# Optimization experiments

Measured on AMD Instinct MI355X. Metric: run time of the kernel, lower is better.

## Reference

```python
import jax, jax.numpy as jnp
import numpy as np

IN_FEATURES = 4096
OUT_FEATURES = 11008
TOKENS = 8


def setup_inputs() -> dict:
    key = jax.random.key(0)
    k_x, k_w, k_s, k_b = jax.random.split(key, 4)
    x = jax.random.normal(k_x, (TOKENS, IN_FEATURES), dtype=jnp.float32)
    # int8-valued quantized weights stored as int32 for portability
    weight_quantized = jax.random.randint(k_w, (OUT_FEATURES, IN_FEATURES), -128, 128, dtype=jnp.int32)
    # per-channel scales (positive, small), shape (out, 1)
    weight_scale = jax.random.uniform(k_s, (OUT_FEATURES, 1), dtype=jnp.float32, minval=1e-4, maxval=2e-2)
    # symmetric quantization -> zero points are zero
    weight_zero_point = jnp.zeros((OUT_FEATURES, 1), dtype=jnp.int32)
    bias = jax.random.normal(k_b, (OUT_FEATURES,), dtype=jnp.float32)
    return {
        "x": x,
        "weight_quantized": weight_quantized,
        "weight_scale": weight_scale,
        "weight_zero_point": weight_zero_point,
        "bias": bias,
    }


def reference(x, weight_quantized, weight_scale, weight_zero_point, bias):
    # Dequantize: (q - zp) * scale, per output channel  -> [out, in] fp32
    w_fp = (weight_quantized.astype(jnp.float32) - weight_zero_point.astype(jnp.float32)) * weight_scale
    # F.linear: x @ W^T + b  -> [tokens, out]
    out = jnp.einsum("ti,oi->to", x, w_fp) + bias
    return out
```

## Files before the change

### kernel.cpp

```cpp
#include <hip/hip_runtime.h>
#include <hip/hip_bf16.h>


constexpr int K_IN  = 4096;
constexpr int N_OUT = 11008;
constexpr int KQ    = K_IN / 4;
constexpr int ITERS = KQ / (64 * 4);

__global__ __launch_bounds__(256) void qlin_kernel(
    const float* __restrict__ x,
    const int*   __restrict__ q,
    const float* __restrict__ scale,
    const int*   __restrict__ zp,
    const float* __restrict__ bias,
    float*       __restrict__ out)
{
    __shared__ float partial[3][64];

    const int tid  = threadIdx.x;
    const int lane = tid & 63;
    const int w    = tid >> 6;
    const int obase = blockIdx.x * 8;
    const int kbase = w * KQ;

    float acc[64];
    #pragma unroll
    for (int i = 0; i < 64; ++i) acc[i] = 0.0f;
    float xs[8];
    #pragma unroll
    for (int t = 0; t < 8; ++t) xs[t] = 0.0f;

    #pragma unroll 2
    for (int it = 0; it < ITERS; ++it) {
        const int k0 = kbase + it * 256 + lane * 4;

        float4 xv[8];
        #pragma unroll
        for (int t = 0; t < 8; ++t)
            xv[t] = *reinterpret_cast<const float4*>(&x[t * K_IN + k0]);

        int4 qv[8];
        #pragma unroll
        for (int c = 0; c < 8; ++c)
            qv[c] = *reinterpret_cast<const int4*>(&q[(obase + c) * K_IN + k0]);

        #pragma unroll
        for (int c = 0; c < 8; ++c) {
            const float q0 = (float)qv[c].x;
            const float q1 = (float)qv[c].y;
            const float q2 = (float)qv[c].z;
            const float q3 = (float)qv[c].w;
            #pragma unroll
            for (int t = 0; t < 8; ++t) {
                acc[t * 8 + c] += xv[t].x * q0 + xv[t].y * q1
                                + xv[t].z * q2 + xv[t].w * q3;
            }
        }
        #pragma unroll
        for (int t = 0; t < 8; ++t)
            xs[t] += xv[t].x + xv[t].y + xv[t].z + xv[t].w;
    }

    #pragma unroll
    for (int s = 0; s < 6; ++s) {
        const int m    = 32 >> s;
        const int half = 32 >> s;
        const bool hi  = (lane & m) != 0;
        #pragma unroll
        for (int i = 0; i < half; ++i) {
            const float a = acc[i];
            const float b = acc[i + half];
            const float send = hi ? a : b;
            const float recv = __shfl_xor(send, m, 64);
            acc[i] = (hi ? b : a) + recv;
        }
    }

    #pragma unroll
    for (int m = 1; m <= 32; m <<= 1) {
        #pragma unroll
        for (int t = 0; t < 8; ++t)
            xs[t] += __shfl_xor(xs[t], m, 64);
    }

    const int t = lane >> 3;
    const int c = lane & 7;
    const int o = obase + c;
    const float v = acc[0] - (float)zp[o] * xs[t];

    if (w != 0)
        partial[w - 1][lane] = v;
    __syncthreads();
    if (w == 0) {
        const float total = v + partial[0][lane] + partial[1][lane] + partial[2][lane];
        out[t * N_OUT + o] = scale[o] * total + bias[o];
    }
}

extern "C" void kernel_launch(void* const* d_in, const int* in_sizes, int n_in,
                              void* d_out, int out_size, void* d_ws, size_t ws_size,
                              hipStream_t stream) {
    const float* x     = (const float*)d_in[0];
    const int*   q     = (const int*)  d_in[1];
    const float* scale = (const float*)d_in[2];
    const int*   zp    = (const int*)  d_in[3];
    const float* bias  = (const float*)d_in[4];
    float* out = (float*)d_out;

    const int blocks = N_OUT / 8;
    qlin_kernel<<<blocks, 256, 0, stream>>>(x, q, scale, zp, bias, out);
}
```

Measured before the change: 43.35 us.

## Split tokens across lanes to shrink accumulators and raise occupancy

Each lane now handles one token (lane&7) and one of 8 k-slots (lane>>3). It keeps only 8 accumulators and one x float4 instead of 64 accumulators and 8 x vectors. This cuts register pressure, and the launch bounds are raised to allow more waves per CU. The reduction shrinks to 3 transpose-shuffle stages plus a 3-step xs reduction. The catch is that the 8 lanes sharing a k-slot load the same int4 weight elements redundantly, so weight loads become less coalesced per lane group, and there are 8x more loop iterations.

Measured after the change: 71.44 us. 64.8% more time.

```diff
diff --git a/kernel.cpp b/kernel.cpp
--- a/kernel.cpp
+++ b/kernel.cpp
@@ -5,9 +5,9 @@
 constexpr int K_IN  = 4096;
 constexpr int N_OUT = 11008;
 constexpr int KQ    = K_IN / 4;
-constexpr int ITERS = KQ / (64 * 4);
+constexpr int ITERS = KQ / 32;
 
-__global__ __launch_bounds__(256) void qlin_kernel(
+__global__ __launch_bounds__(256, 8) void qlin_kernel(
     const float* __restrict__ x,
     const int*   __restrict__ q,
     const float* __restrict__ scale,
@@ -20,24 +20,22 @@
     const int tid  = threadIdx.x;
     const int lane = tid & 63;
     const int w    = tid >> 6;
+    const int t    = lane & 7;
+    const int s    = lane >> 3;
     const int obase = blockIdx.x * 8;
     const int kbase = w * KQ;
 
-    float acc[64];
+    const float* xrow = x + t * K_IN;
+
+    float acc[8];
     #pragma unroll
-    for (int i = 0; i < 64; ++i) acc[i] = 0.0f;
-    float xs[8];
-    #pragma unroll
-    for (int t = 0; t < 8; ++t) xs[t] = 0.0f;
+    for (int c = 0; c < 8; ++c) acc[c] = 0.0f;
+    float xs = 0.0f;
 
-    #pragma unroll 2
     for (int it = 0; it < ITERS; ++it) {
-        const int k0 = kbase + it * 256 + lane * 4;
+        const int k0 = kbase + it * 32 + s * 4;
 
-        float4 xv[8];
-        #pragma unroll
-        for (int t = 0; t < 8; ++t)
-            xv[t] = *reinterpret_cast<const float4*>(&x[t * K_IN + k0]);
+        const float4 xv = *reinterpret_cast<const float4*>(&xrow[k0]);
 
         int4 qv[8];
         #pragma unroll
@@ -46,25 +44,16 @@
 
         #pragma unroll
         for (int c = 0; c < 8; ++c) {
-            const float q0 = (float)qv[c].x;
-            const float q1 = (float)qv[c].y;
-            const float q2 = (float)qv[c].z;
-            const float q3 = (float)qv[c].w;
-            #pragma unroll
-            for (int t = 0; t < 8; ++t) {
-                acc[t * 8 + c] += xv[t].x * q0 + xv[t].y * q1
-                                + xv[t].z * q2 + xv[t].w * q3;
-            }
+            acc[c] += xv.x * (float)qv[c].x + xv.y * (float)qv[c].y
+                    + xv.z * (float)qv[c].z + xv.w * (float)qv[c].w;
         }
-        #pragma unroll
-        for (int t = 0; t < 8; ++t)
-            xs[t] += xv[t].x + xv[t].y + xv[t].z + xv[t].w;
+        xs += xv.x + xv.y + xv.z + xv.w;
     }
 
     #pragma unroll
-    for (int s = 0; s < 6; ++s) {
-        const int m    = 32 >> s;
-        const int half = 32 >> s;
+    for (int st = 0; st < 3; ++st) {
+        const int m    = 32 >> st;
+        const int half = 4 >> st;
         const bool hi  = (lane & m) != 0;
         #pragma unroll
         for (int i = 0; i < half; ++i) {
@@ -77,16 +66,11 @@
     }
 
     #pragma unroll
-    for (int m = 1; m <= 32; m <<= 1) {
-        #pragma unroll
-        for (int t = 0; t < 8; ++t)
-            xs[t] += __shfl_xor(xs[t], m, 64);
-    }
+    for (int m = 8; m <= 32; m <<= 1)
+        xs += __shfl_xor(xs, m, 64);
 
-    const int t = lane >> 3;
-    const int c = lane & 7;
-    const int o = obase + c;
-    const float v = acc[0] - (float)zp[o] * xs[t];
+    const int o = obase + s;
+    const float v = acc[0] - (float)zp[o] * xs;
 
     if (w != 0)
         partial[w - 1][lane] = v;
```

## Split work across tokens and channel groups instead of K-splitting per block

Applied to the files above, without the earlier changes.

Each block now covers 16 output channels. Its four waves are split into two channel groups of 8 and two token halves of 4, and every wave walks the full K dimension instead of a quarter of it. This removes the shared-memory partial reduction and __syncthreads, halves the per-thread accumulator count, and adds a launch-bounds occupancy hint. The cost is that each weight row is now read by two waves (one per token half), which doubles L1/L2 traffic on the int32 weights. Each wave also runs a longer serial K loop.

Measured after the change: 46.22 us. +6.6%, slower.

```diff
diff --git a/kernel.cpp b/kernel.cpp
--- a/kernel.cpp
+++ b/kernel.cpp
@@ -4,10 +4,9 @@
 
 constexpr int K_IN  = 4096;
 constexpr int N_OUT = 11008;
-constexpr int KQ    = K_IN / 4;
-constexpr int ITERS = KQ / (64 * 4);
+constexpr int ITERS = K_IN / 256;
 
-__global__ __launch_bounds__(256) void qlin_kernel(
+__global__ __launch_bounds__(256, 4) void qlin_kernel(
     const float* __restrict__ x,
     const int*   __restrict__ q,
     const float* __restrict__ scale,
@@ -15,29 +14,27 @@
     const float* __restrict__ bias,
     float*       __restrict__ out)
 {
-    __shared__ float partial[3][64];
-
     const int tid  = threadIdx.x;
     const int lane = tid & 63;
     const int w    = tid >> 6;
-    const int obase = blockIdx.x * 8;
-    const int kbase = w * KQ;
+    const int th   = w & 1;
+    const int cg   = w >> 1;
+    const int obase = blockIdx.x * 16 + cg * 8;
+    const int tbase = th * 4;
 
-    float acc[64];
+    float acc[32];
     #pragma unroll
-    for (int i = 0; i < 64; ++i) acc[i] = 0.0f;
-    float xs[8];
-    #pragma unroll
-    for (int t = 0; t < 8; ++t) xs[t] = 0.0f;
+    for (int i = 0; i < 32; ++i) acc[i] = 0.0f;
+    float xs[4] = {0.0f, 0.0f, 0.0f, 0.0f};
 
     #pragma unroll 2
     for (int it = 0; it < ITERS; ++it) {
-        const int k0 = kbase + it * 256 + lane * 4;
+        const int k0 = it * 256 + lane * 4;
 
-        float4 xv[8];
+        float4 xv[4];
         #pragma unroll
-        for (int t = 0; t < 8; ++t)
-            xv[t] = *reinterpret_cast<const float4*>(&x[t * K_IN + k0]);
+        for (int t = 0; t < 4; ++t)
+            xv[t] = *reinterpret_cast<const float4*>(&x[(tbase + t) * K_IN + k0]);
 
         int4 qv[8];
         #pragma unroll
@@ -51,20 +48,20 @@
             const float q2 = (float)qv[c].z;
             const float q3 = (float)qv[c].w;
             #pragma unroll
-            for (int t = 0; t < 8; ++t) {
+            for (int t = 0; t < 4; ++t) {
                 acc[t * 8 + c] += xv[t].x * q0 + xv[t].y * q1
                                 + xv[t].z * q2 + xv[t].w * q3;
             }
         }
         #pragma unroll
-        for (int t = 0; t < 8; ++t)
+        for (int t = 0; t < 4; ++t)
             xs[t] += xv[t].x + xv[t].y + xv[t].z + xv[t].w;
     }
 
     #pragma unroll
-    for (int s = 0; s < 6; ++s) {
-        const int m    = 32 >> s;
-        const int half = 32 >> s;
+    for (int st = 0; st < 5; ++st) {
+        const int m    = 32 >> st;
+        const int half = 16 >> st;
         const bool hi  = (lane & m) != 0;
         #pragma unroll
         for (int i = 0; i < half; ++i) {
@@ -75,25 +72,22 @@
             acc[i] = (hi ? b : a) + recv;
         }
     }
+    acc[0] += __shfl_xor(acc[0], 1, 64);
 
     #pragma unroll
     for (int m = 1; m <= 32; m <<= 1) {
         #pragma unroll
-        for (int t = 0; t < 8; ++t)
+        for (int t = 0; t < 4; ++t)
             xs[t] += __shfl_xor(xs[t], m, 64);
     }
 
-    const int t = lane >> 3;
-    const int c = lane & 7;
-    const int o = obase + c;
-    const float v = acc[0] - (float)zp[o] * xs[t];
-
-    if (w != 0)
-        partial[w - 1][lane] = v;
-    __syncthreads();
-    if (w == 0) {
-        const float total = v + partial[0][lane] + partial[1][lane] + partial[2][lane];
-        out[t * N_OUT + o] = scale[o] * total + bias[o];
+    const int j  = lane >> 1;
+    const int tl = j >> 3;
+    const int c  = j & 7;
+    const int o  = obase + c;
+    if ((lane & 1) == 0) {
+        const float total = acc[0] - (float)zp[o] * xs[tl];
+        out[(tbase + tl) * N_OUT + o] = scale[o] * total + bias[o];
     }
 }
 
@@ -107,6 +101,6 @@
     const float* bias  = (const float*)d_in[4];
     float* out = (float*)d_out;
 
-    const int blocks = N_OUT / 8;
+    const int blocks = N_OUT / 16;
     qlin_kernel<<<blocks, 256, 0, stream>>>(x, q, scale, zp, bias, out);
 }
```
